# Kernel optimization log

Hardware: AMD Instinct MI355X
Metric: run time of the kernel (lower is better)

The kernel has to match this reference:

```python
import jax, jax.numpy as jnp
import numpy as np

B, N, K = 4, 65536, 16
D_IN, D_OUT = 8, 16
DH = D_OUT // 2
GROUPS = 4  # GroupNorm: 4 groups since all channel counts here are < 64
NEG = 0.2   # LeakyReLU negative slope
EPS = 1e-5  # GroupNorm eps (torch default)


def _gather(feat, idx):
    # feat [B,C,N], idx [B,N,K] -> [B,C,N,K]  (gather_neighbour_V2)
    return jax.vmap(lambda f, i: f[:, i])(feat, idx)


def _gn(x, gamma, beta):
    b, c, n, k = x.shape
    xg = x.reshape(b, GROUPS, c // GROUPS, n, k)
    mu = xg.mean(axis=(2, 3, 4), keepdims=True)
    var = xg.var(axis=(2, 3, 4), keepdims=True)
    xg = (xg - mu) * jax.lax.rsqrt(var + EPS)
    return xg.reshape(b, c, n, k) * gamma[None, :, None, None] + beta[None, :, None, None]


def _mlp2d(x, W, bb, g, be, act=True):
    # Conv2d 1x1 (+bias) + GroupNorm + optional LeakyReLU(0.2)
    y = jnp.einsum('oc,bcnk->bonk', W, x) + bb[None, :, None, None]
    y = _gn(y, g, be)
    return jax.nn.leaky_relu(y, NEG) if act else y


def _att_pool(x, Wa, Wm, bm, gm, bem):
    # Att_pooling: 1x1 fc (no bias) -> softmax over nsample -> weighted sum -> MLP2D
    scores = jax.nn.softmax(jnp.einsum('oc,bcnk->bonk', Wa, x), axis=3)
    agg = jnp.sum(x * scores, axis=3, keepdims=True)  # [B,C,N,1]
    return _mlp2d(agg, Wm, bm, gm, bem)


def setup_inputs():
    key = jax.random.key(0)
    ks = list(jax.random.split(key, 16))
    def w(k, o, c):
        return jax.random.normal(k, (o, c), jnp.float32) * (2.0 / c) ** 0.5  # kaiming-ish
    inp = {
        'feature': jax.random.normal(ks[0], (B, D_IN, N, 1), jnp.float32),
        'xyz': jax.random.normal(ks[1], (B, 3, N), jnp.float32),
        'neigh_idx': jax.random.randint(ks[2], (B, N, K), 0, N),
        'W_mlp1': w(ks[3], DH, D_IN), 'b_mlp1': jnp.zeros(DH), 'g_mlp1': jnp.ones(DH), 'be_mlp1': jnp.zeros(DH),
        'W_lfa1': w(ks[4], DH, 10), 'b_lfa1': jnp.zeros(DH), 'g_lfa1': jnp.ones(DH), 'be_lfa1': jnp.zeros(DH),
        'Wa1': w(ks[5], D_OUT, D_OUT),
        'Wm1': w(ks[6], DH, D_OUT), 'bm1': jnp.zeros(DH), 'gm1': jnp.ones(DH), 'bem1': jnp.zeros(DH),
        'W_lfa2': w(ks[7], DH, DH), 'b_lfa2': jnp.zeros(DH), 'g_lfa2': jnp.ones(DH), 'be_lfa2': jnp.zeros(DH),
        'Wa2': w(ks[8], D_OUT, D_OUT),
        'Wm2': w(ks[9], D_OUT, D_OUT), 'bm2': jnp.zeros(D_OUT), 'gm2': jnp.ones(D_OUT), 'bem2': jnp.zeros(D_OUT),
        'W_mlp2': w(ks[10], 2 * D_OUT, D_OUT), 'b_mlp2': jnp.zeros(2 * D_OUT), 'g_mlp2': jnp.ones(2 * D_OUT), 'be_mlp2': jnp.zeros(2 * D_OUT),
        'W_skip': w(ks[11], 2 * D_OUT, D_IN), 'b_skip': jnp.zeros(2 * D_OUT), 'g_skip': jnp.ones(2 * D_OUT), 'be_skip': jnp.zeros(2 * D_OUT),
    }
    return inp


def reference(feature, xyz, neigh_idx,
              W_mlp1, b_mlp1, g_mlp1, be_mlp1,
              W_lfa1, b_lfa1, g_lfa1, be_lfa1,
              Wa1, Wm1, bm1, gm1, bem1,
              W_lfa2, b_lfa2, g_lfa2, be_lfa2,
              Wa2, Wm2, bm2, gm2, bem2,
              W_mlp2, b_mlp2, g_mlp2, be_mlp2,
              W_skip, b_skip, g_skip, be_skip):
    # Dilated_res_block.forward
    f_pc = _mlp2d(feature, W_mlp1, b_mlp1, g_mlp1, be_mlp1)          # [B,DH,N,1]
    # Building_block.relative_pos_encoding
    neigh_xyz = _gather(xyz, neigh_idx)                               # [B,3,N,K]
    xyz_tile = xyz[:, :, :, None]
    rel = neigh_xyz - xyz_tile
    dist = jnp.sqrt(jnp.sum(rel * rel, axis=1, keepdims=True))        # [B,1,N,K]
    f_rel = jnp.concatenate(
        [dist, rel, jnp.broadcast_to(xyz_tile, neigh_xyz.shape), neigh_xyz], axis=1)  # [B,10,N,K]
    f_xyz = _mlp2d(f_rel, W_lfa1, b_lfa1, g_lfa1, be_lfa1)            # [B,DH,N,K]
    f_neigh = _gather(f_pc[..., 0], neigh_idx)                        # [B,DH,N,K]
    f_concat = jnp.concatenate([f_neigh, f_xyz], axis=1)              # [B,D_OUT,N,K]
    f_agg = _att_pool(f_concat, Wa1, Wm1, bm1, gm1, bem1)             # [B,DH,N,1]
    f_xyz2 = _mlp2d(f_xyz, W_lfa2, b_lfa2, g_lfa2, be_lfa2)           # [B,DH,N,K]
    f_neigh2 = _gather(f_agg[..., 0], neigh_idx)                      # [B,DH,N,K]
    f_concat2 = jnp.concatenate([f_neigh2, f_xyz2], axis=1)           # [B,D_OUT,N,K]
    f_agg2 = _att_pool(f_concat2, Wa2, Wm2, bm2, gm2, bem2)           # [B,D_OUT,N,1]
    f_out = _mlp2d(f_agg2, W_mlp2, b_mlp2, g_mlp2, be_mlp2, act=False)    # [B,2*D_OUT,N,1]
    shortcut = _mlp2d(feature, W_skip, b_skip, g_skip, be_skip, act=False)
    return jax.nn.leaky_relu(f_out + shortcut, NEG)
```

## Files before the change

### kernel.cpp

```cpp
#include <hip/hip_runtime.h>
#include <hip/hip_bf16.h>

#define NPTS 65536
#define LOGN 16
#define KNB 16
#define NEGS 0.2f
#define EPSV 1e-5f

#define ST_MLP1 0
#define ST_SKIP 1
#define ST_L1   2
#define ST_M1   3
#define ST_L2   4
#define ST_M2   5
#define ST_OUT  6

#define STAT_F   14336
#define FIN_OFF  14336
#define RECA_OFF 16384
#define RECB_OFF (RECA_OFF + 4*NPTS*8)
#define PREM2_OFF (RECB_OFF + 4*NPTS*8)

typedef __attribute__((ext_vector_type(8))) short short8;
typedef __attribute__((ext_vector_type(4))) float f32x4;

union U16 { uint4 u; short8 s; };

__device__ __forceinline__ float lrelu(float v){ return fmaxf(v, v*NEGS); }

__device__ __forceinline__ float s16(float v){ return v + __shfl_xor(v,16); }
__device__ __forceinline__ float s32(float v){ return v + __shfl_xor(v,32); }
__device__ __forceinline__ float x16max(float v){ return fmaxf(v, __shfl_xor(v,16)); }
__device__ __forceinline__ float x32max(float v){ return fmaxf(v, __shfl_xor(v,32)); }

__device__ __forceinline__ float wred(float v){
  #pragma unroll
  for(int off=32; off>0; off>>=1) v += __shfl_xor(v, off, 64);
  return v;
}

__device__ __forceinline__ void wave_fence(){
  __builtin_amdgcn_sched_barrier(0);
  asm volatile("s_waitcnt lgkmcnt(0)" ::: "memory");
  __builtin_amdgcn_sched_barrier(0);
}

__device__ __forceinline__ void load_fin(const float* fin, int stage, int b, int c,
                                         float& sc, float& sh){
  const float* fp = fin + ((stage*4+b)*32 + c)*2;
  sc = fp[0]; sh = fp[1];
}

__device__ __forceinline__ unsigned pkbf(float a, float b){
  __hip_bfloat162 h = __float22bfloat162_rn(make_float2(a,b));
  union{ __hip_bfloat162 h2; unsigned u; } cv; cv.h2 = h; return cv.u;
}
__device__ __forceinline__ float blo(unsigned d){ return __builtin_bit_cast(float, d<<16); }
__device__ __forceinline__ float bhi(unsigned d){ return __builtin_bit_cast(float, d & 0xffff0000u); }
__device__ __forceinline__ float bfu(unsigned short h){ return __builtin_bit_cast(float, ((unsigned)h)<<16); }

__device__ __forceinline__ int rowadr(int row){ return (row*16) ^ ((row&8)<<2); }

#define XB_OFF 0
#define AG_OFF 2048
#define WV_BYTES 2304

__device__ __forceinline__ void xcd_map(int bid, int& b, int& nblk){
  int xcd = bid & 7;
  b = xcd >> 1;
  nblk = ((bid >> 3) << 1) | (xcd & 1);
}

__global__ __launch_bounds__(256) void k_pack(const float* __restrict__ xyz,
                                              float* __restrict__ ws){
  int p = blockIdx.x*256 + threadIdx.x;
  int b = p >> LOGN, n = p & (NPTS-1);
  const float* xb = xyz + b*3*NPTS + n;
  float4 v = make_float4(xb[0], xb[NPTS], xb[2*NPTS], 0.f);
  *(float4*)((char*)(ws + RECA_OFF) + (size_t)p*32 + 16) = v;
  *(float4*)((char*)(ws + RECB_OFF) + (size_t)p*32 + 16) = v;
}

__device__ void fin_stage(const float* __restrict__ ws, float* __restrict__ fin,
                          int stage, int nch, float cnt,
                          const float* __restrict__ gamma, const float* __restrict__ beta){
  int t = threadIdx.x;
  if(t >= 4*nch) return;
  int b = t / nch, c = t - b*nch;
  int g = c / (nch/4);
  const float* sl = ws + ((stage*4+b)*4+g)*128;
  float s=0.f, q=0.f;
  #pragma unroll 8
  for(int i=0;i<64;i++){ s += sl[i]; q += sl[64+i]; }
  float mean = s/cnt;
  float var  = q/cnt - mean*mean;
  float inv  = rsqrtf(var + EPSV);
  float sc = inv*gamma[c];
  float sh = beta[c] - mean*sc;
  float* fp = fin + ((stage*4+b)*32 + c)*2;
  fp[0]=sc; fp[1]=sh;
}

__global__ __launch_bounds__(128) void kfA(float* __restrict__ ws,
    const float* g1, const float* be1, const float* gL1, const float* beL1,
    const float* gsk, const float* besk){
  if(blockIdx.x==0)      fin_stage(ws, ws+FIN_OFF, ST_MLP1, 8,  2.0f*NPTS,      g1, be1);
  else if(blockIdx.x==1) fin_stage(ws, ws+FIN_OFF, ST_L1,   8,  2.0f*NPTS*KNB,  gL1, beL1);
  else                   fin_stage(ws, ws+FIN_OFF, ST_SKIP, 32, 8.0f*NPTS,      gsk, besk);
}
__global__ __launch_bounds__(128) void kfB(float* __restrict__ ws,
    const float* gm1, const float* bem1, const float* gL2, const float* beL2){
  if(blockIdx.x==0) fin_stage(ws, ws+FIN_OFF, ST_M1, 8, 2.0f*NPTS,     gm1, bem1);
  else              fin_stage(ws, ws+FIN_OFF, ST_L2, 8, 2.0f*NPTS*KNB, gL2, beL2);
}
__global__ __launch_bounds__(128) void kfC(float* __restrict__ ws,
    const float* gm2, const float* bem2){
  fin_stage(ws, ws+FIN_OFF, ST_M2, 16, 4.0f*NPTS, gm2, bem2);
}
__global__ __launch_bounds__(128) void kfD(float* __restrict__ ws,
    const float* go, const float* beo){
  fin_stage(ws, ws+FIN_OFF, ST_OUT, 32, 8.0f*NPTS, go, beo);
}

__global__ __launch_bounds__(256) void k1(
    const float* __restrict__ feat, const int* __restrict__ nidx,
    const float* __restrict__ W1,  const float* __restrict__ b1,
    const float* __restrict__ Ws,  const float* __restrict__ bs,
    const float* __restrict__ WL1, const float* __restrict__ bl1,
    float* __restrict__ ws){
  int b, nblk; xcd_map(blockIdx.x, b, nblk);
  int n = nblk*256 + threadIdx.x;
  int p = (b<<LOGN) | n;
  char* recA = (char*)(ws + RECA_OFF);
  float f[8];
  #pragma unroll
  for(int c=0;c<8;c++) f[c] = feat[(b*8+c)*NPTS + n];

  float s1s[4]={0,0,0,0}, s1q[4]={0,0,0,0};
  float pv[8];
  #pragma unroll
  for(int c=0;c<8;c++){
    float v = b1[c];
    #pragma unroll
    for(int j=0;j<8;j++) v += W1[c*8+j]*f[j];
    pv[c]=v;
    s1s[c>>1]+=v; s1q[c>>1]+=v*v;
  }
  uint4 pk = make_uint4(pkbf(pv[0],pv[1]), pkbf(pv[2],pv[3]),
                        pkbf(pv[4],pv[5]), pkbf(pv[6],pv[7]));
  *(uint4*)(recA + (size_t)p*32) = pk;

  float sss[4]={0,0,0,0}, ssq[4]={0,0,0,0};
  #pragma unroll
  for(int o=0;o<32;o++){
    float v = bs[o];
    #pragma unroll
    for(int j=0;j<8;j++) v += Ws[o*8+j]*f[j];
    sss[o>>3]+=v; ssq[o>>3]+=v*v;
  }
  float4 ct = *(const float4*)(recA + (size_t)p*32 + 16);
  float l1s[4]={0,0,0,0}, l1q[4]={0,0,0,0};
  const int* nr = nidx + p*KNB;
  #pragma unroll
  for(int k=0;k<KNB;k++){
    int idx = nr[k];
    float4 nb = *(const float4*)(recA + ((size_t)((b<<LOGN)|idx))*32 + 16);
    float rx=nb.x-ct.x, ry=nb.y-ct.y, rz=nb.z-ct.z;
    float dd = __builtin_amdgcn_sqrtf(rx*rx+ry*ry+rz*rz);
    float fr[10] = {dd,rx,ry,rz,ct.x,ct.y,ct.z,nb.x,nb.y,nb.z};
    #pragma unroll
    for(int c=0;c<8;c++){
      float v = bl1[c];
      #pragma unroll
      for(int j=0;j<10;j++) v += WL1[c*10+j]*fr[j];
      l1s[c>>1]+=v; l1q[c>>1]+=v*v;
    }
  }
  __shared__ float lst[24];
  if(threadIdx.x < 24) lst[threadIdx.x] = 0.f;
  __syncthreads();
  int lane = threadIdx.x & 63;
  #pragma unroll
  for(int g=0; g<4; g++){
    float a1v = wred(s1s[g]), a2v = wred(s1q[g]);
    float d1v = wred(sss[g]), d2v = wred(ssq[g]);
    float e1v = wred(l1s[g]), e2v = wred(l1q[g]);
    if(lane==0){
      atomicAdd(&lst[ 0+g*2], a1v); atomicAdd(&lst[ 1+g*2], a2v);
      atomicAdd(&lst[ 8+g*2], d1v); atomicAdd(&lst[ 9+g*2], d2v);
      atomicAdd(&lst[16+g*2], e1v); atomicAdd(&lst[17+g*2], e2v);
    }
  }
  __syncthreads();
  if(threadIdx.x < 24){
    int stage = threadIdx.x >> 3;
    int g = (threadIdx.x >> 1) & 3;
    int w = threadIdx.x & 1;
    atomicAdd(ws + ((stage*4+b)*4+g)*128 + w*64 + (blockIdx.x&63), lst[threadIdx.x]);
  }
}

__global__ __launch_bounds__(256,8) void k2(
    const int* __restrict__ nidx,
    const float* __restrict__ WL1, const float* __restrict__ bl1,
    const float* __restrict__ Wa1,
    const float* __restrict__ Wm1, const float* __restrict__ bm1,
    const float* __restrict__ W2,  const float* __restrict__ b2,
    float* __restrict__ ws){
  const float* fin = ws + FIN_OFF;
  int b, nblk; xcd_map(blockIdx.x, b, nblk);
  int tid = threadIdx.x;
  int w = tid>>6, lane = tid&63, q = lane>>4, l15 = lane&15;
  int nbase = nblk*16 + w*4;
  int pA = (b<<LOGN) | (nbase + q);

  float scP[8], shP[8], scL[8], shL[8];
  #pragma unroll
  for(int c=0;c<8;c++){
    load_fin(fin, ST_MLP1,b,c, scP[c],shP[c]);
    load_fin(fin, ST_L1,  b,c, scL[c],shL[c]);
  }
  U16 bu; bu.u = make_uint4(0,0,0,0);
  if(q < 2){
    const float* wr = Wa1 + l15*16 + q*8;
    float4 w0 = *(const float4*)(wr);
    float4 w1 = *(const float4*)(wr+4);
    bu.u = make_uint4(pkbf(w0.x,w0.y), pkbf(w0.z,w0.w), pkbf(w1.x,w1.y), pkbf(w1.z,w1.w));
  }

  __shared__ unsigned char SB[4][WV_BYTES];
  __shared__ float lst[16];
  if(tid<16) lst[tid]=0.f;
  char* wb = (char*)SB[w];

  char* recA = (char*)(ws + RECA_OFF);
  char* recB = (char*)(ws + RECB_OFF);

  int idx = nidx[pA*KNB + l15];
  const char* rp = recA + ((size_t)((b<<LOGN)|idx))*32;
  uint4 pk1  = *(const uint4*)(rp);
  float4 nb  = *(const float4*)(rp + 16);
  float4 ct  = *(const float4*)(recA + (size_t)pA*32 + 16);
  float rx=nb.x-ct.x, ry=nb.y-ct.y, rz=nb.z-ct.z;
  float dd = __builtin_amdgcn_sqrtf(rx*rx+ry*ry+rz*rz);
  float fr[10] = {dd,rx,ry,rz,ct.x,ct.y,ct.z,nb.x,nb.y,nb.z};
  float fx[8];
  #pragma unroll
  for(int c=0;c<8;c++){
    float v = bl1[c];
    #pragma unroll
    for(int j=0;j<10;j++) v += WL1[c*10+j]*fr[j];
    fx[c] = lrelu(v*scL[c]+shL[c]);
  }
  float xn[8];
  xn[0]=lrelu(blo(pk1.x)*scP[0]+shP[0]); xn[1]=lrelu(bhi(pk1.x)*scP[1]+shP[1]);
  xn[2]=lrelu(blo(pk1.y)*scP[2]+shP[2]); xn[3]=lrelu(bhi(pk1.y)*scP[3]+shP[3]);
  xn[4]=lrelu(blo(pk1.z)*scP[4]+shP[4]); xn[5]=lrelu(bhi(pk1.z)*scP[5]+shP[5]);
  xn[6]=lrelu(blo(pk1.w)*scP[6]+shP[6]); xn[7]=lrelu(bhi(pk1.w)*scP[7]+shP[7]);

  {
    uint4 d0 = make_uint4(pkbf(xn[0],xn[1]), pkbf(xn[2],xn[3]), pkbf(xn[4],xn[5]), pkbf(xn[6],xn[7]));
    uint4 d1 = make_uint4(pkbf(fx[0],fx[1]), pkbf(fx[2],fx[3]), pkbf(fx[4],fx[5]), pkbf(fx[6],fx[7]));
    char* base = wb + XB_OFF + q*256 + rowadr(l15);
    *(uint4*)(base)        = d0;
    *(uint4*)(base + 1024) = d1;
  }

  wave_fence();

  f32x4 cz = {0.f,0.f,0.f,0.f};
  int rxf = q & 2;
  const char* xc = wb + XB_OFF + (l15>>3)*1024 + (l15&7)*2;
  #pragma unroll
  for(int pt=0; pt<4; pt++){
    U16 afr; afr.u = make_uint4(0,0,0,0);
    if(q < 2) afr.u = *(const uint4*)(wb + XB_OFF + q*1024 + pt*256 + rowadr(l15));
    f32x4 cf = __builtin_amdgcn_mfma_f32_16x16x32_bf16(afr.s, bu.s, cz, 0,0,0);
    float mx = fmaxf(fmaxf(cf[0],cf[1]), fmaxf(cf[2],cf[3]));
    mx = x16max(mx); mx = x32max(mx);
    float pe0=__expf(cf[0]-mx), pe1=__expf(cf[1]-mx), pe2=__expf(cf[2]-mx), pe3=__expf(cf[3]-mx);
    float ps = pe0+pe1+pe2+pe3;
    ps = s16(ps); ps = s32(ps);
    const char* xe = xc + pt*256 + 64*q;
    float acc = pe0*bfu(*(const unsigned short*)(xe + 16*(0^rxf)))
              + pe1*bfu(*(const unsigned short*)(xe + 16*(1^rxf)))
              + pe2*bfu(*(const unsigned short*)(xe + 16*(2^rxf)))
              + pe3*bfu(*(const unsigned short*)(xe + 16*(3^rxf)));
    acc = s16(acc); acc = s32(acc);
    float agg = acc*__builtin_amdgcn_rcpf(ps);
    if(q==0) *(float*)(wb + AG_OFF + (pt*16+l15)*4) = agg;
  }

  float l2s[4]={0,0,0,0}, l2q[4]={0,0,0,0};
  #pragma unroll
  for(int c=0;c<8;c++){
    float v = b2[c];
    #pragma unroll
    for(int j=0;j<8;j++) v += W2[c*8+j]*fx[j];
    l2s[c>>1]+=v; l2q[c>>1]+=v*v;
  }

  wave_fence();

  float m1v = 0.f;
  if(l15 < 8){
    const float4* agp = (const float4*)(wb + AG_OFF + q*64);
    float4 A0=agp[0], A1=agp[1], A2=agp[2], A3=agp[3];
    const float4* wp = (const float4*)(Wm1 + l15*16);
    float4 W0=wp[0], W1_=wp[1], W2_=wp[2], W3=wp[3];
    float v = bm1[l15];
    v += W0.x*A0.x + W0.y*A0.y + W0.z*A0.z + W0.w*A0.w;
    v += W1_.x*A1.x + W1_.y*A1.y + W1_.z*A1.z + W1_.w*A1.w;
    v += W2_.x*A2.x + W2_.y*A2.y + W2_.z*A2.z + W2_.w*A2.w;
    v += W3.x*A3.x + W3.y*A3.y + W3.z*A3.z + W3.w*A3.w;
    m1v = v;
  }
  float vpart = __shfl_xor(m1v, 1);
  if(l15 < 8 && (l15&1)==0){
    unsigned u = pkbf(m1v, vpart);
    int pD = (b<<LOGN) | (nbase + q);
    *(unsigned*)(recB + (size_t)pD*32 + (l15>>1)*4) = u;
  }
  float m1s = s16(m1v); m1s = s32(m1s); m1s += __shfl_xor(m1s,1);
  float m1qv = m1v*m1v;
  float m1q = s16(m1qv); m1q = s32(m1q); m1q += __shfl_xor(m1q,1);

  __syncthreads();
  #pragma unroll
  for(int g=0;g<4;g++){
    float a=wred(l2s[g]), qq=wred(l2q[g]);
    if(lane==0){ atomicAdd(&lst[g*2],a); atomicAdd(&lst[g*2+1],qq); }
  }
  if(lane < 8 && (lane&1)==0){
    atomicAdd(&lst[8+(lane>>1)*2],   m1s);
    atomicAdd(&lst[8+(lane>>1)*2+1], m1q);
  }
  __syncthreads();
  if(tid<16){
    int half=tid>>3, g=(tid>>1)&3, wsel=tid&1;
    int stage = half? ST_M1 : ST_L2;
    atomicAdd(ws + ((stage*4+b)*4+g)*128 + wsel*64 + (blockIdx.x&63), lst[tid]);
  }
}

__global__ __launch_bounds__(256,8) void k3(
    const int* __restrict__ nidx,
    const float* __restrict__ WL1, const float* __restrict__ bl1,
    const float* __restrict__ W2,  const float* __restrict__ b2,
    const float* __restrict__ Wa2,
    const float* __restrict__ Wm2, const float* __restrict__ bm2,
    float* __restrict__ ws){
  const float* fin = ws + FIN_OFF;
  int b, nblk; xcd_map(blockIdx.x, b, nblk);
  int tid = threadIdx.x;
  int w = tid>>6, lane = tid&63, q = lane>>4, l15 = lane&15;
  int nbase = nblk*16 + w*4;
  int pA = (b<<LOGN) | (nbase + q);

  float scL[8], shL[8], scL2[8], shL2[8], scM[8], shM[8];
  #pragma unroll
  for(int c=0;c<8;c++){
    load_fin(fin, ST_L1, b,c, scL[c], shL[c]);
    load_fin(fin, ST_L2, b,c, scL2[c],shL2[c]);
    load_fin(fin, ST_M1, b,c, scM[c], shM[c]);
  }
  U16 bu; bu.u = make_uint4(0,0,0,0);
  if(q < 2){
    const float* wr = Wa2 + l15*16 + q*8;
    float4 w0 = *(const float4*)(wr);
    float4 w1 = *(const float4*)(wr+4);
    bu.u = make_uint4(pkbf(w0.x,w0.y), pkbf(w0.z,w0.w), pkbf(w1.x,w1.y), pkbf(w1.z,w1.w));
  }
  float wmr[16];
  {
    const float4* wp = (const float4*)(Wm2 + l15*16);
    float4 m0=wp[0], m1=wp[1], m2=wp[2], m3=wp[3];
    wmr[0]=m0.x; wmr[1]=m0.y; wmr[2]=m0.z; wmr[3]=m0.w;
    wmr[4]=m1.x; wmr[5]=m1.y; wmr[6]=m1.z; wmr[7]=m1.w;
    wmr[8]=m2.x; wmr[9]=m2.y; wmr[10]=m2.z; wmr[11]=m2.w;
    wmr[12]=m3.x; wmr[13]=m3.y; wmr[14]=m3.z; wmr[15]=m3.w;
  }

  __shared__ unsigned char SB[4][WV_BYTES];
  __shared__ float lst[8];
  if(tid<8) lst[tid]=0.f;
  char* wb = (char*)SB[w];

  char* recB = (char*)(ws + RECB_OFF);
  float* prem2 = ws + PREM2_OFF;

  int idx = nidx[pA*KNB + l15];
  const char* rp = recB + ((size_t)((b<<LOGN)|idx))*32;
  uint4 pm1 = *(const uint4*)(rp);
  float4 nb = *(const float4*)(rp + 16);
  float4 ct = *(const float4*)(recB + (size_t)pA*32 + 16);
  float rx=nb.x-ct.x, ry=nb.y-ct.y, rz=nb.z-ct.z;
  float dd = __builtin_amdgcn_sqrtf(rx*rx+ry*ry+rz*rz);
  float fr[10] = {dd,rx,ry,rz,ct.x,ct.y,ct.z,nb.x,nb.y,nb.z};
  float fx[8];
  #pragma unroll
  for(int c=0;c<8;c++){
    float v = bl1[c];
    #pragma unroll
    for(int j=0;j<10;j++) v += WL1[c*10+j]*fr[j];
    fx[c] = lrelu(v*scL[c]+shL[c]);
  }
  float fx2[8];
  #pragma unroll
  for(int c=0;c<8;c++){
    float v = b2[c];
    #pragma unroll
    for(int j=0;j<8;j++) v += W2[c*8+j]*fx[j];
    fx2[c] = lrelu(v*scL2[c]+shL2[c]);
  }
  float xn[8];
  xn[0]=lrelu(blo(pm1.x)*scM[0]+shM[0]); xn[1]=lrelu(bhi(pm1.x)*scM[1]+shM[1]);
  xn[2]=lrelu(blo(pm1.y)*scM[2]+shM[2]); xn[3]=lrelu(bhi(pm1.y)*scM[3]+shM[3]);
  xn[4]=lrelu(blo(pm1.z)*scM[4]+shM[4]); xn[5]=lrelu(bhi(pm1.z)*scM[5]+shM[5]);
  xn[6]=lrelu(blo(pm1.w)*scM[6]+shM[6]); xn[7]=lrelu(bhi(pm1.w)*scM[7]+shM[7]);

  {
    uint4 d0 = make_uint4(pkbf(xn[0],xn[1]), pkbf(xn[2],xn[3]), pkbf(xn[4],xn[5]), pkbf(xn[6],xn[7]));
    uint4 d1 = make_uint4(pkbf(fx2[0],fx2[1]), pkbf(fx2[2],fx2[3]), pkbf(fx2[4],fx2[5]), pkbf(fx2[6],fx2[7]));
    char* base = wb + XB_OFF + q*256 + rowadr(l15);
    *(uint4*)(base)        = d0;
    *(uint4*)(base + 1024) = d1;
  }

  wave_fence();

  f32x4 cz = {0.f,0.f,0.f,0.f};
  int rxf = q & 2;
  const char* xc = wb + XB_OFF + (l15>>3)*1024 + (l15&7)*2;
  #pragma unroll
  for(int pt=0; pt<4; pt++){
    U16 afr; afr.u = make_uint4(0,0,0,0);
    if(q < 2) afr.u = *(const uint4*)(wb + XB_OFF + q*1024 + pt*256 + rowadr(l15));
    f32x4 cf = __builtin_amdgcn_mfma_f32_16x16x32_bf16(afr.s, bu.s, cz, 0,0,0);
    float mx = fmaxf(fmaxf(cf[0],cf[1]), fmaxf(cf[2],cf[3]));
    mx = x16max(mx); mx = x32max(mx);
    float pe0=__expf(cf[0]-mx), pe1=__expf(cf[1]-mx), pe2=__expf(cf[2]-mx), pe3=__expf(cf[3]-mx);
    float ps = pe0+pe1+pe2+pe3;
    ps = s16(ps); ps = s32(ps);
    const char* xe = xc + pt*256 + 64*q;
    float acc = pe0*bfu(*(const unsigned short*)(xe + 16*(0^rxf)))
              + pe1*bfu(*(const unsigned short*)(xe + 16*(1^rxf)))
              + pe2*bfu(*(const unsigned short*)(xe + 16*(2^rxf)))
              + pe3*bfu(*(const unsigned short*)(xe + 16*(3^rxf)));
    acc = s16(acc); acc = s32(acc);
    float agg = acc*__builtin_amdgcn_rcpf(ps);
    if(q==0) *(float*)(wb + AG_OFF + (pt*16+l15)*4) = agg;
  }

  wave_fence();

  float v;
  {
    const float4* agp = (const float4*)(wb + AG_OFF + q*64);
    float4 A0=agp[0], A1=agp[1], A2=agp[2], A3=agp[3];
    v = bm2[l15];
    v += wmr[0]*A0.x + wmr[1]*A0.y + wmr[2]*A0.z + wmr[3]*A0.w;
    v += wmr[4]*A1.x + wmr[5]*A1.y + wmr[6]*A1.z + wmr[7]*A1.w;
    v += wmr[8]*A2.x + wmr[9]*A2.y + wmr[10]*A2.z + wmr[11]*A2.w;
    v += wmr[12]*A3.x + wmr[13]*A3.y + wmr[14]*A3.z + wmr[15]*A3.w;
  }
  int pD = (b<<LOGN) | (nbase + q);
  prem2[(size_t)pD*16 + l15] = v;

  float s = s16(v);  s = s32(s);  s += __shfl_xor(s,1);  s += __shfl_xor(s,2);
  float qv = v*v;
  float qq = s16(qv); qq = s32(qq); qq += __shfl_xor(qq,1); qq += __shfl_xor(qq,2);

  __syncthreads();
  if(lane < 16 && (lane&3)==0){
    atomicAdd(&lst[(lane>>2)*2],   s);
    atomicAdd(&lst[(lane>>2)*2+1], qq);
  }
  __syncthreads();
  if(tid<8){
    int g=(tid>>1)&3, wsel=tid&1;
    atomicAdd(ws + ((ST_M2*4+b)*4+g)*128 + wsel*64 + (blockIdx.x&63), lst[tid]);
  }
}

__global__ __launch_bounds__(256) void k4(
    const float* __restrict__ Wo,  const float* __restrict__ bo,
    float* __restrict__ ws){
  const float* fin = ws + FIN_OFF;
  int b=blockIdx.y; int n=blockIdx.x*256+threadIdx.x; int p=(b<<LOGN)|n;
  float scM[16], shM[16];
  #pragma unroll
  for(int c=0;c<16;c++) load_fin(fin, ST_M2, b, c, scM[c], shM[c]);
  const float4* pm = (const float4*)(ws + PREM2_OFF) + (size_t)p*4;
  float fa[16];
  #pragma unroll
  for(int i=0;i<4;i++){
    float4 v4 = pm[i];
    fa[i*4+0]=lrelu(v4.x*scM[i*4+0]+shM[i*4+0]);
    fa[i*4+1]=lrelu(v4.y*scM[i*4+1]+shM[i*4+1]);
    fa[i*4+2]=lrelu(v4.z*scM[i*4+2]+shM[i*4+2]);
    fa[i*4+3]=lrelu(v4.w*scM[i*4+3]+shM[i*4+3]);
  }
  float sos[4]={0,0,0,0}, soq[4]={0,0,0,0};
  #pragma unroll
  for(int o=0;o<32;o++){
    float v=bo[o];
    #pragma unroll
    for(int c=0;c<16;c++) v += Wo[o*16+c]*fa[c];
    sos[o>>3]+=v; soq[o>>3]+=v*v;
  }
  __shared__ float lst[8];
  if(threadIdx.x<8) lst[threadIdx.x]=0.f;
  __syncthreads();
  int lane = threadIdx.x & 63;
  #pragma unroll
  for(int g=0;g<4;g++){
    float a=wred(sos[g]), q=wred(soq[g]);
    if(lane==0){ atomicAdd(&lst[g*2],a); atomicAdd(&lst[g*2+1],q); }
  }
  __syncthreads();
  if(threadIdx.x<8){
    int g=(threadIdx.x>>1)&3, w=threadIdx.x&1;
    atomicAdd(ws + ((ST_OUT*4+b)*4+g)*128 + w*64 + (blockIdx.x&63), lst[threadIdx.x]);
  }
}

__global__ __launch_bounds__(256) void k5(
    const float* __restrict__ feat,
    const float* __restrict__ Wo,  const float* __restrict__ bo,
    const float* __restrict__ Wsk, const float* __restrict__ bsk,
    const float* __restrict__ ws, float* __restrict__ out){
  const float* fin = ws + FIN_OFF;
  int b=blockIdx.y; int n=blockIdx.x*256+threadIdx.x; int p=(b<<LOGN)|n;
  float scM[16], shM[16];
  #pragma unroll
  for(int c=0;c<16;c++) load_fin(fin, ST_M2, b, c, scM[c], shM[c]);
  const float4* pm = (const float4*)(ws + PREM2_OFF) + (size_t)p*4;
  float fa[16];
  #pragma unroll
  for(int i=0;i<4;i++){
    float4 v4 = pm[i];
    fa[i*4+0]=lrelu(v4.x*scM[i*4+0]+shM[i*4+0]);
    fa[i*4+1]=lrelu(v4.y*scM[i*4+1]+shM[i*4+1]);
    fa[i*4+2]=lrelu(v4.z*scM[i*4+2]+shM[i*4+2]);
    fa[i*4+3]=lrelu(v4.w*scM[i*4+3]+shM[i*4+3]);
  }
  float f[8];
  #pragma unroll
  for(int c=0;c<8;c++) f[c]=feat[(b*8+c)*NPTS+n];
  #pragma unroll
  for(int o=0;o<32;o++){
    float to = bo[o];
    #pragma unroll
    for(int c=0;c<16;c++) to += Wo[o*16+c]*fa[c];
    float ts = bsk[o];
    #pragma unroll
    for(int j=0;j<8;j++) ts += Wsk[o*8+j]*f[j];
    float scO, shO, scS, shS;
    load_fin(fin, ST_OUT,  b, o, scO, shO);
    load_fin(fin, ST_SKIP, b, o, scS, shS);
    float v = to*scO+shO + ts*scS+shS;
    out[(b*32+o)*NPTS + n] = lrelu(v);
  }
}

extern "C" void kernel_launch(void* const* d_in, const int* in_sizes, int n_in,
                              void* d_out, int out_size, void* d_ws, size_t ws_size,
                              hipStream_t stream){
  (void)in_sizes; (void)n_in; (void)out_size; (void)ws_size;
  const float* feat=(const float*)d_in[0];
  const float* xyz =(const float*)d_in[1];
  const int*   nidx=(const int*)d_in[2];
  const float* W1  =(const float*)d_in[3];
  const float* b1  =(const float*)d_in[4];
  const float* g1  =(const float*)d_in[5];
  const float* be1 =(const float*)d_in[6];
  const float* WL1 =(const float*)d_in[7];
  const float* bl1 =(const float*)d_in[8];
  const float* gL1 =(const float*)d_in[9];
  const float* beL1=(const float*)d_in[10];
  const float* Wa1 =(const float*)d_in[11];
  const float* Wm1 =(const float*)d_in[12];
  const float* bm1 =(const float*)d_in[13];
  const float* gm1 =(const float*)d_in[14];
  const float* bem1=(const float*)d_in[15];
  const float* W2  =(const float*)d_in[16];
  const float* b2  =(const float*)d_in[17];
  const float* gL2 =(const float*)d_in[18];
  const float* beL2=(const float*)d_in[19];
  const float* Wa2 =(const float*)d_in[20];
  const float* Wm2 =(const float*)d_in[21];
  const float* bm2 =(const float*)d_in[22];
  const float* gm2 =(const float*)d_in[23];
  const float* bem2=(const float*)d_in[24];
  const float* Wo  =(const float*)d_in[25];
  const float* bo  =(const float*)d_in[26];
  const float* go  =(const float*)d_in[27];
  const float* beo =(const float*)d_in[28];
  const float* Wsk =(const float*)d_in[29];
  const float* bsk =(const float*)d_in[30];
  const float* gsk =(const float*)d_in[31];
  const float* besk=(const float*)d_in[32];
  float* ws=(float*)d_ws;
  float* out=(float*)d_out;

  hipMemsetAsync(d_ws, 0, STAT_F*sizeof(float), stream);
  k_pack<<<dim3(1024),dim3(256),0,stream>>>(xyz, ws);
  k1<<<dim3(1024),dim3(256),0,stream>>>(feat, nidx, W1,b1, Wsk,bsk, WL1,bl1, ws);
  kfA<<<dim3(3),dim3(128),0,stream>>>(ws, g1,be1, gL1,beL1, gsk,besk);
  k2<<<dim3(16384),dim3(256),0,stream>>>(nidx, WL1,bl1, Wa1, Wm1,bm1, W2,b2, ws);
  kfB<<<dim3(2),dim3(128),0,stream>>>(ws, gm1,bem1, gL2,beL2);
  k3<<<dim3(16384),dim3(256),0,stream>>>(nidx, WL1,bl1, W2,b2, Wa2, Wm2,bm2, ws);
  kfC<<<dim3(1),dim3(128),0,stream>>>(ws, gm2,bem2);
  k4<<<dim3(256,4),dim3(256),0,stream>>>(Wo,bo, ws);
  kfD<<<dim3(1),dim3(128),0,stream>>>(ws, go,beo);
  k5<<<dim3(256,4),dim3(256),0,stream>>>(feat, Wo,bo, Wsk,bsk, ws, out);
}
```

Baseline: 285.4 us.

## Materialize lfa2 pre-norm values in k2 and reuse in k3; add nontemporal accesses

k2 now stores the pre-GroupNorm lfa2 output (bf16, 16 bytes per point-neighbour) to a new workspace region when the workspace is large enough. k3 then reads it back instead of recomputing the relative-xyz features and both small MLPs from the gathered neighbour coordinates. Streaming loads and stores of feat, nidx, prem2 and out are also marked nontemporal to reduce cache pollution. The trade is about 64 MB of extra write plus read traffic against removed recompute and scattered gather loads, and the path is chosen at runtime from ws_size.

After: 261.9 us. 8.2% less time.

```diff
diff --git a/kernel.cpp b/kernel.cpp
--- a/kernel.cpp
+++ b/kernel.cpp
@@ -18,11 +18,15 @@
 #define STAT_F   14336
 #define FIN_OFF  14336
 #define RECA_OFF 16384
-#define RECB_OFF (RECA_OFF + 4*NPTS*8)
+#define RECB_OFF  (RECA_OFF + 4*NPTS*8)
 #define PREM2_OFF (RECB_OFF + 4*NPTS*8)
+#define L2P_OFF   (PREM2_OFF + 4*NPTS*16)
+#define L2P_FLOATS ((size_t)4*NPTS*KNB*4)
+#define NEED_BYTES (((size_t)L2P_OFF + L2P_FLOATS)*4)
 
 typedef __attribute__((ext_vector_type(8))) short short8;
 typedef __attribute__((ext_vector_type(4))) float f32x4;
+typedef __attribute__((ext_vector_type(4))) unsigned u32x4;
 
 union U16 { uint4 u; short8 s; };
 
@@ -134,7 +138,7 @@
   char* recA = (char*)(ws + RECA_OFF);
   float f[8];
   #pragma unroll
-  for(int c=0;c<8;c++) f[c] = feat[(b*8+c)*NPTS + n];
+  for(int c=0;c<8;c++) f[c] = __builtin_nontemporal_load(feat + (b*8+c)*NPTS + n);
 
   float s1s[4]={0,0,0,0}, s1q[4]={0,0,0,0};
   float pv[8];
@@ -163,7 +167,7 @@
   const int* nr = nidx + p*KNB;
   #pragma unroll
   for(int k=0;k<KNB;k++){
-    int idx = nr[k];
+    int idx = __builtin_nontemporal_load(nr + k);
     float4 nb = *(const float4*)(recA + ((size_t)((b<<LOGN)|idx))*32 + 16);
     float rx=nb.x-ct.x, ry=nb.y-ct.y, rz=nb.z-ct.z;
     float dd = __builtin_amdgcn_sqrtf(rx*rx+ry*ry+rz*rz);
@@ -200,6 +204,7 @@
   }
 }
 
+template<bool L2P>
 __global__ __launch_bounds__(256,8) void k2(
     const int* __restrict__ nidx,
     const float* __restrict__ WL1, const float* __restrict__ bl1,
@@ -236,7 +241,7 @@
   char* recA = (char*)(ws + RECA_OFF);
   char* recB = (char*)(ws + RECB_OFF);
 
-  int idx = nidx[pA*KNB + l15];
+  int idx = __builtin_nontemporal_load(nidx + (size_t)pA*KNB + l15);
   const char* rp = recA + ((size_t)((b<<LOGN)|idx))*32;
   uint4 pk1  = *(const uint4*)(rp);
   float4 nb  = *(const float4*)(rp + 16);
@@ -264,6 +269,20 @@
     char* base = wb + XB_OFF + q*256 + rowadr(l15);
     *(uint4*)(base)        = d0;
     *(uint4*)(base + 1024) = d1;
+  }
+
+  float l2v[8];
+  #pragma unroll
+  for(int c=0;c<8;c++){
+    float v = b2[c];
+    #pragma unroll
+    for(int j=0;j<8;j++) v += W2[c*8+j]*fx[j];
+    l2v[c]=v;
+  }
+  if constexpr (L2P){
+    u32x4 lp = { pkbf(l2v[0],l2v[1]), pkbf(l2v[2],l2v[3]),
+                 pkbf(l2v[4],l2v[5]), pkbf(l2v[6],l2v[7]) };
+    __builtin_nontemporal_store(lp, (u32x4*)((char*)(ws + L2P_OFF) + ((size_t)pA*KNB + l15)*16));
   }
 
   wave_fence();
@@ -293,12 +312,7 @@
 
   float l2s[4]={0,0,0,0}, l2q[4]={0,0,0,0};
   #pragma unroll
-  for(int c=0;c<8;c++){
-    float v = b2[c];
-    #pragma unroll
-    for(int j=0;j<8;j++) v += W2[c*8+j]*fx[j];
-    l2s[c>>1]+=v; l2q[c>>1]+=v*v;
-  }
+  for(int c=0;c<8;c++){ l2s[c>>1]+=l2v[c]; l2q[c>>1]+=l2v[c]*l2v[c]; }
 
   wave_fence();
 
@@ -343,6 +357,7 @@
   }
 }
 
+template<bool L2P>
 __global__ __launch_bounds__(256,8) void k3(
     const int* __restrict__ nidx,
     const float* __restrict__ WL1, const float* __restrict__ bl1,
@@ -389,29 +404,38 @@
   char* recB = (char*)(ws + RECB_OFF);
   float* prem2 = ws + PREM2_OFF;
 
-  int idx = nidx[pA*KNB + l15];
+  int idx = __builtin_nontemporal_load(nidx + (size_t)pA*KNB + l15);
   const char* rp = recB + ((size_t)((b<<LOGN)|idx))*32;
   uint4 pm1 = *(const uint4*)(rp);
-  float4 nb = *(const float4*)(rp + 16);
-  float4 ct = *(const float4*)(recB + (size_t)pA*32 + 16);
-  float rx=nb.x-ct.x, ry=nb.y-ct.y, rz=nb.z-ct.z;
-  float dd = __builtin_amdgcn_sqrtf(rx*rx+ry*ry+rz*rz);
-  float fr[10] = {dd,rx,ry,rz,ct.x,ct.y,ct.z,nb.x,nb.y,nb.z};
-  float fx[8];
-  #pragma unroll
-  for(int c=0;c<8;c++){
-    float v = bl1[c];
-    #pragma unroll
-    for(int j=0;j<10;j++) v += WL1[c*10+j]*fr[j];
-    fx[c] = lrelu(v*scL[c]+shL[c]);
-  }
   float fx2[8];
-  #pragma unroll
-  for(int c=0;c<8;c++){
-    float v = b2[c];
-    #pragma unroll
-    for(int j=0;j<8;j++) v += W2[c*8+j]*fx[j];
-    fx2[c] = lrelu(v*scL2[c]+shL2[c]);
+  if constexpr (L2P){
+    u32x4 lp = __builtin_nontemporal_load(
+        (const u32x4*)((const char*)(ws + L2P_OFF) + ((size_t)pA*KNB + l15)*16));
+    fx2[0]=lrelu(blo(lp.x)*scL2[0]+shL2[0]); fx2[1]=lrelu(bhi(lp.x)*scL2[1]+shL2[1]);
+    fx2[2]=lrelu(blo(lp.y)*scL2[2]+shL2[2]); fx2[3]=lrelu(bhi(lp.y)*scL2[3]+shL2[3]);
+    fx2[4]=lrelu(blo(lp.z)*scL2[4]+shL2[4]); fx2[5]=lrelu(bhi(lp.z)*scL2[5]+shL2[5]);
+    fx2[6]=lrelu(blo(lp.w)*scL2[6]+shL2[6]); fx2[7]=lrelu(bhi(lp.w)*scL2[7]+shL2[7]);
+  } else {
+    float4 nb = *(const float4*)(rp + 16);
+    float4 ct = *(const float4*)(recB + (size_t)pA*32 + 16);
+    float rx=nb.x-ct.x, ry=nb.y-ct.y, rz=nb.z-ct.z;
+    float dd = __builtin_amdgcn_sqrtf(rx*rx+ry*ry+rz*rz);
+    float fr[10] = {dd,rx,ry,rz,ct.x,ct.y,ct.z,nb.x,nb.y,nb.z};
+    float fx[8];
+    #pragma unroll
+    for(int c=0;c<8;c++){
+      float v = bl1[c];
+      #pragma unroll
+      for(int j=0;j<10;j++) v += WL1[c*10+j]*fr[j];
+      fx[c] = lrelu(v*scL[c]+shL[c]);
+    }
+    #pragma unroll
+    for(int c=0;c<8;c++){
+      float v = b2[c];
+      #pragma unroll
+      for(int j=0;j<8;j++) v += W2[c*8+j]*fx[j];
+      fx2[c] = lrelu(v*scL2[c]+shL2[c]);
+    }
   }
   float xn[8];
   xn[0]=lrelu(blo(pm1.x)*scM[0]+shM[0]); xn[1]=lrelu(bhi(pm1.x)*scM[1]+shM[1]);
@@ -465,7 +489,7 @@
     v += wmr[12]*A3.x + wmr[13]*A3.y + wmr[14]*A3.z + wmr[15]*A3.w;
   }
   int pD = (b<<LOGN) | (nbase + q);
-  prem2[(size_t)pD*16 + l15] = v;
+  __builtin_nontemporal_store(v, prem2 + (size_t)pD*16 + l15);
 
   float s = s16(v);  s = s32(s);  s += __shfl_xor(s,1);  s += __shfl_xor(s,2);
   float qv = v*v;
@@ -491,11 +515,11 @@
   float scM[16], shM[16];
   #pragma unroll
   for(int c=0;c<16;c++) load_fin(fin, ST_M2, b, c, scM[c], shM[c]);
-  const float4* pm = (const float4*)(ws + PREM2_OFF) + (size_t)p*4;
+  const f32x4* pm = (const f32x4*)(ws + PREM2_OFF) + (size_t)p*4;
   float fa[16];
   #pragma unroll
   for(int i=0;i<4;i++){
-    float4 v4 = pm[i];
+    f32x4 v4 = __builtin_nontemporal_load(pm + i);
     fa[i*4+0]=lrelu(v4.x*scM[i*4+0]+shM[i*4+0]);
     fa[i*4+1]=lrelu(v4.y*scM[i*4+1]+shM[i*4+1]);
     fa[i*4+2]=lrelu(v4.z*scM[i*4+2]+shM[i*4+2]);
@@ -535,11 +559,11 @@
   float scM[16], shM[16];
   #pragma unroll
   for(int c=0;c<16;c++) load_fin(fin, ST_M2, b, c, scM[c], shM[c]);
-  const float4* pm = (const float4*)(ws + PREM2_OFF) + (size_t)p*4;
+  const f32x4* pm = (const f32x4*)(ws + PREM2_OFF) + (size_t)p*4;
   float fa[16];
   #pragma unroll
   for(int i=0;i<4;i++){
-    float4 v4 = pm[i];
+    f32x4 v4 = __builtin_nontemporal_load(pm + i);
     fa[i*4+0]=lrelu(v4.x*scM[i*4+0]+shM[i*4+0]);
     fa[i*4+1]=lrelu(v4.y*scM[i*4+1]+shM[i*4+1]);
     fa[i*4+2]=lrelu(v4.z*scM[i*4+2]+shM[i*4+2]);
@@ -547,7 +571,7 @@
   }
   float f[8];
   #pragma unroll
-  for(int c=0;c<8;c++) f[c]=feat[(b*8+c)*NPTS+n];
+  for(int c=0;c<8;c++) f[c]=__builtin_nontemporal_load(feat + (b*8+c)*NPTS + n);
   #pragma unroll
   for(int o=0;o<32;o++){
     float to = bo[o];
@@ -560,14 +584,14 @@
     load_fin(fin, ST_OUT,  b, o, scO, shO);
     load_fin(fin, ST_SKIP, b, o, scS, shS);
     float v = to*scO+shO + ts*scS+shS;
-    out[(b*32+o)*NPTS + n] = lrelu(v);
+    __builtin_nontemporal_store(lrelu(v), out + (size_t)(b*32+o)*NPTS + n);
   }
 }
 
 extern "C" void kernel_launch(void* const* d_in, const int* in_sizes, int n_in,
                               void* d_out, int out_size, void* d_ws, size_t ws_size,
                               hipStream_t stream){
-  (void)in_sizes; (void)n_in; (void)out_size; (void)ws_size;
+  (void)in_sizes; (void)n_in; (void)out_size;
   const float* feat=(const float*)d_in[0];
   const float* xyz =(const float*)d_in[1];
   const int*   nidx=(const int*)d_in[2];
@@ -604,13 +628,21 @@
   float* ws=(float*)d_ws;
   float* out=(float*)d_out;
 
+  bool useL2P = (ws_size >= NEED_BYTES);
+
   hipMemsetAsync(d_ws, 0, STAT_F*sizeof(float), stream);
   k_pack<<<dim3(1024),dim3(256),0,stream>>>(xyz, ws);
   k1<<<dim3(1024),dim3(256),0,stream>>>(feat, nidx, W1,b1, Wsk,bsk, WL1,bl1, ws);
   kfA<<<dim3(3),dim3(128),0,stream>>>(ws, g1,be1, gL1,beL1, gsk,besk);
-  k2<<<dim3(16384),dim3(256),0,stream>>>(nidx, WL1,bl1, Wa1, Wm1,bm1, W2,b2, ws);
+  if(useL2P)
+    k2<true><<<dim3(16384),dim3(256),0,stream>>>(nidx, WL1,bl1, Wa1, Wm1,bm1, W2,b2, ws);
+  else
+    k2<false><<<dim3(16384),dim3(256),0,stream>>>(nidx, WL1,bl1, Wa1, Wm1,bm1, W2,b2, ws);
   kfB<<<dim3(2),dim3(128),0,stream>>>(ws, gm1,bem1, gL2,beL2);
-  k3<<<dim3(16384),dim3(256),0,stream>>>(nidx, WL1,bl1, W2,b2, Wa2, Wm2,bm2, ws);
+  if(useL2P)
+    k3<true><<<dim3(16384),dim3(256),0,stream>>>(nidx, WL1,bl1, W2,b2, Wa2, Wm2,bm2, ws);
+  else
+    k3<false><<<dim3(16384),dim3(256),0,stream>>>(nidx, WL1,bl1, W2,b2, Wa2, Wm2,bm2, ws);
   kfC<<<dim3(1),dim3(128),0,stream>>>(ws, gm2,bem2);
   k4<<<dim3(256,4),dim3(256),0,stream>>>(Wo,bo, ws);
   kfD<<<dim3(1),dim3(128),0,stream>>>(ws, go,beo);
```
